# Kernel optimization log

Hardware: AMD Instinct MI355X
Metric: run time of the kernel (lower is better)

Reference implementation:

```python
import jax, jax.numpy as jnp
import numpy as np

CH = 96          # channels
E = 2 * CH       # expand_ratio * channels = 192
S = 16           # ssm_state_dim
LN_EPS = 1e-3    # keras LayerNormalization default epsilon


def setup_inputs() -> dict:
    key = jax.random.key(0)
    ks = jax.random.split(key, 8)
    inputs = jax.random.normal(ks[0], (8, 128, 128, CH), dtype=jnp.float32)
    scale = 0.05
    return {
        "inputs": inputs,
        "ln_gamma": jnp.ones((CH,), jnp.float32),
        "ln_beta": jnp.zeros((CH,), jnp.float32),
        "W_expand": jax.random.normal(ks[1], (CH, E), jnp.float32) * scale,
        "W_gate": jax.random.normal(ks[2], (CH, E), jnp.float32) * scale,
        "A": jax.random.normal(ks[3], (E, S), jnp.float32) * scale,
        "B": jax.random.normal(ks[4], (E, S), jnp.float32) * scale,
        "C": jax.random.normal(ks[5], (E, S), jnp.float32) * scale,
        "D": jnp.zeros((E,), jnp.float32),
        "W_out": jax.random.normal(ks[6], (E, CH), jnp.float32) * scale,
    }


def _layernorm(x, gamma, beta):
    mean = jnp.mean(x, axis=-1, keepdims=True)
    var = jnp.mean(jnp.square(x - mean), axis=-1, keepdims=True)
    return (x - mean) / jnp.sqrt(var + LN_EPS) * gamma + beta


def _ssm_scan(u, A, B, C, D):
    # u: [Bn, H, W, E]; diagonal linear recurrence along W with per-(channel,state) params.
    Bn, H, W, Ech = u.shape
    u_t = jnp.moveaxis(u, 2, 0)  # [W, Bn, H, E]

    def step(state, u_w):  # state: [Bn, H, E, S], u_w: [Bn, H, E]
        st = state * A + u_w[..., None] * B               # [Bn, H, E, S]
        # Faithful to the TF code: u*D is broadcast over the state dim
        # before the sum, contributing S * u * D.
        y = jnp.sum(st * C, axis=-1) + S * u_w * D        # [Bn, H, E]
        return st, y

    init = jnp.zeros((Bn, H, Ech, S), dtype=u.dtype)
    _, y = jax.lax.scan(step, init, u_t)                  # y: [W, Bn, H, E]
    return jnp.moveaxis(y, 0, 2)                          # [Bn, H, W, E]


def reference(inputs, ln_gamma, ln_beta, W_expand, W_gate, A, B, C, D, W_out):
    x = _layernorm(inputs, ln_gamma, ln_beta)
    x_proj = jnp.einsum("bhwc,ce->bhwe", x, W_expand)
    gate = jax.nn.sigmoid(jnp.einsum("bhwc,ce->bhwe", x, W_gate))
    ssm_out = _ssm_scan(x_proj, A, B, C, D)
    gated = gate * ssm_out
    return jnp.einsum("bhwe,ec->bhwc", gated, W_out)
```

## Files before the change

### kernel.cpp

```cpp
#include <hip/hip_runtime.h>
#include <math.h>

#define CHN 96
#define EC 192
#define SS 16
#define WPIX 128
#define TILE 16
#define NTILES (WPIX / TILE)
#define NT 192

__global__ __launch_bounds__(NT, 4)
void mamba_fused(const float* __restrict__ in,
                 const float* __restrict__ gamma,
                 const float* __restrict__ beta,
                 const float* __restrict__ We,
                 const float* __restrict__ Wg,
                 const float* __restrict__ Ap,
                 const float* __restrict__ Bp,
                 const float* __restrict__ Cp,
                 const float* __restrict__ Dp,
                 const float* __restrict__ Wo,
                 float* __restrict__ out) {
    __shared__ float xs[TILE][CHN];
    __shared__ float gs[TILE][EC];
    __shared__ float gsm[CHN], bsm[CHN];

    const int t = threadIdx.x;
    const int row = blockIdx.x;
    const float* inrow = in + (size_t)row * WPIX * CHN;

    if (t < CHN) { gsm[t] = gamma[t]; bsm[t] = beta[t]; }

    const int e = t;
    float Ar[SS], Br[SS], Cr[SS], st[SS];
    const float d = Dp[e];
    #pragma unroll
    for (int s4 = 0; s4 < SS / 4; ++s4) {
        float4 a = *(const float4*)&Ap[e * SS + s4 * 4];
        float4 b = *(const float4*)&Bp[e * SS + s4 * 4];
        float4 c = *(const float4*)&Cp[e * SS + s4 * 4];
        Ar[s4*4+0]=a.x; Ar[s4*4+1]=a.y; Ar[s4*4+2]=a.z; Ar[s4*4+3]=a.w;
        Br[s4*4+0]=b.x; Br[s4*4+1]=b.y; Br[s4*4+2]=b.z; Br[s4*4+3]=b.w;
        Cr[s4*4+0]=c.x; Cr[s4*4+1]=c.y; Cr[s4*4+2]=c.z; Cr[s4*4+3]=c.w;
    }
    #pragma unroll
    for (int s = 0; s < SS; ++s) st[s] = 0.f;

    const int px = t >> 3;
    const int ln = t & 7;
    const int co  = t % CHN;
    const int wgr = t / CHN;

    __syncthreads();

    for (int tile = 0; tile < NTILES; ++tile) {
        const int w0 = tile * TILE;

        if (t < 128) {
            const float* pin = inrow + (size_t)(w0 + px) * CHN + ln * 12;
            float4 v0 = *(const float4*)(pin + 0);
            float4 v1 = *(const float4*)(pin + 4);
            float4 v2 = *(const float4*)(pin + 8);
            float sum = v0.x + v0.y + v0.z + v0.w
                      + v1.x + v1.y + v1.z + v1.w
                      + v2.x + v2.y + v2.z + v2.w;
            float sq = v0.x*v0.x + v0.y*v0.y + v0.z*v0.z + v0.w*v0.w
                     + v1.x*v1.x + v1.y*v1.y + v1.z*v1.z + v1.w*v1.w
                     + v2.x*v2.x + v2.y*v2.y + v2.z*v2.z + v2.w*v2.w;
            #pragma unroll
            for (int m = 1; m < 8; m <<= 1) {
                sum += __shfl_xor(sum, m);
                sq  += __shfl_xor(sq,  m);
            }
            const float mean = sum * (1.f / CHN);
            const float var  = sq * (1.f / CHN) - mean * mean;
            const float rstd = rsqrtf(var + 1e-3f);
            const int cb = ln * 12;
            float o[12] = {v0.x,v0.y,v0.z,v0.w, v1.x,v1.y,v1.z,v1.w, v2.x,v2.y,v2.z,v2.w};
            #pragma unroll
            for (int k = 0; k < 12; ++k)
                o[k] = (o[k] - mean) * rstd * gsm[cb + k] + bsm[cb + k];
            *(float4*)&xs[px][cb + 0] = make_float4(o[0], o[1], o[2],  o[3]);
            *(float4*)&xs[px][cb + 4] = make_float4(o[4], o[5], o[6],  o[7]);
            *(float4*)&xs[px][cb + 8] = make_float4(o[8], o[9], o[10], o[11]);
        }
        __syncthreads();

        float accp[TILE], accg[TILE];
        #pragma unroll
        for (int w = 0; w < TILE; ++w) { accp[w] = 0.f; accg[w] = 0.f; }

        for (int c4 = 0; c4 < CHN / 4; ++c4) {
            const int c = c4 * 4;
            const float we0 = We[(c + 0) * EC + e];
            const float we1 = We[(c + 1) * EC + e];
            const float we2 = We[(c + 2) * EC + e];
            const float we3 = We[(c + 3) * EC + e];
            const float wg0 = Wg[(c + 0) * EC + e];
            const float wg1 = Wg[(c + 1) * EC + e];
            const float wg2 = Wg[(c + 2) * EC + e];
            const float wg3 = Wg[(c + 3) * EC + e];
            #pragma unroll
            for (int w = 0; w < TILE; ++w) {
                float4 xv = *(const float4*)&xs[w][c];
                accp[w] = fmaf(xv.x, we0, accp[w]);
                accp[w] = fmaf(xv.y, we1, accp[w]);
                accp[w] = fmaf(xv.z, we2, accp[w]);
                accp[w] = fmaf(xv.w, we3, accp[w]);
                accg[w] = fmaf(xv.x, wg0, accg[w]);
                accg[w] = fmaf(xv.y, wg1, accg[w]);
                accg[w] = fmaf(xv.z, wg2, accg[w]);
                accg[w] = fmaf(xv.w, wg3, accg[w]);
            }
        }

        #pragma unroll
        for (int w = 0; w < TILE; ++w) {
            const float u = accp[w];
            float y = (float)SS * u * d;
            #pragma unroll
            for (int s = 0; s < SS; ++s) {
                st[s] = fmaf(st[s], Ar[s], u * Br[s]);
                y = fmaf(st[s], Cr[s], y);
            }
            const float g = 1.f / (1.f + expf(-accg[w]));
            gs[w][e] = g * y;
        }
        __syncthreads();

        {
            float acco[8];
            #pragma unroll
            for (int j = 0; j < 8; ++j) acco[j] = 0.f;

            for (int e4 = 0; e4 < EC / 4; ++e4) {
                const int ee = e4 * 4;
                const float wo0 = Wo[(ee + 0) * CHN + co];
                const float wo1 = Wo[(ee + 1) * CHN + co];
                const float wo2 = Wo[(ee + 2) * CHN + co];
                const float wo3 = Wo[(ee + 3) * CHN + co];
                #pragma unroll
                for (int j = 0; j < 8; ++j) {
                    float4 gv = *(const float4*)&gs[wgr * 8 + j][ee];
                    acco[j] = fmaf(gv.x, wo0, acco[j]);
                    acco[j] = fmaf(gv.y, wo1, acco[j]);
                    acco[j] = fmaf(gv.z, wo2, acco[j]);
                    acco[j] = fmaf(gv.w, wo3, acco[j]);
                }
            }
            #pragma unroll
            for (int j = 0; j < 8; ++j) {
                out[((size_t)row * WPIX + w0 + wgr * 8 + j) * CHN + co] = acco[j];
            }
        }
        __syncthreads();
    }
}

extern "C" void kernel_launch(void* const* d_in, const int* in_sizes, int n_in,
                              void* d_out, int out_size, void* d_ws, size_t ws_size,
                              hipStream_t stream) {
    const float* in    = (const float*)d_in[0];
    const float* gamma = (const float*)d_in[1];
    const float* beta  = (const float*)d_in[2];
    const float* We    = (const float*)d_in[3];
    const float* Wg    = (const float*)d_in[4];
    const float* Ap    = (const float*)d_in[5];
    const float* Bp    = (const float*)d_in[6];
    const float* Cp    = (const float*)d_in[7];
    const float* Dp    = (const float*)d_in[8];
    const float* Wo    = (const float*)d_in[9];
    float* out = (float*)d_out;

    mamba_fused<<<dim3(8 * 128), dim3(NT), 0, stream>>>(
        in, gamma, beta, We, Wg, Ap, Bp, Cp, Dp, Wo, out);
}
```

Measured before the change: 438.3 us.

## Fold LayerNorm affine into projection weights and pipeline weight loads

Two small prep kernels pre-scale W_expand and W_gate by gamma and precompute per-channel column sums and beta terms. The fused kernel can then apply the normalization as a per-pixel rstd/mean correction after the matmul instead of normalizing every element. The projection now reads raw inputs straight from global memory (relying on cache broadcast) rather than staging normalized values in LDS. Weight loads for both matmuls are double-buffered in registers, the trailing barrier is dropped, the sigmoid uses __expf, and launch bounds drop to 3 waves. The trade-offs are repeated global/L1 reads of the input tile in place of LDS, higher register pressure, and slightly different rounding from the algebraic fold.

```diff
diff --git a/kernel.cpp b/kernel.cpp
--- a/kernel.cpp
+++ b/kernel.cpp
@@ -9,31 +9,98 @@
 #define NTILES (WPIX / TILE)
 #define NT 192
 
-__global__ __launch_bounds__(NT, 4)
+__global__ void prep_scale(const float* __restrict__ We,
+                           const float* __restrict__ Wg,
+                           const float* __restrict__ gamma,
+                           float* __restrict__ WeP,
+                           float* __restrict__ WgP) {
+    const int c = blockIdx.x;
+    const int e = threadIdx.x;
+    const float g = gamma[c];
+    WeP[c * EC + e] = g * We[c * EC + e];
+    WgP[c * EC + e] = g * Wg[c * EC + e];
+}
+
+__global__ void prep_sums(const float* __restrict__ We,
+                          const float* __restrict__ Wg,
+                          const float* __restrict__ beta,
+                          const float* __restrict__ WeP,
+                          const float* __restrict__ WgP,
+                          float* __restrict__ se, float* __restrict__ be,
+                          float* __restrict__ sg, float* __restrict__ bg) {
+    const int e = threadIdx.x;
+    float s1 = 0.f, b1 = 0.f, s2 = 0.f, b2 = 0.f;
+    for (int c = 0; c < CHN; ++c) {
+        s1 += WeP[c * EC + e];
+        s2 += WgP[c * EC + e];
+        b1 += beta[c] * We[c * EC + e];
+        b2 += beta[c] * Wg[c * EC + e];
+    }
+    se[e] = s1; be[e] = b1; sg[e] = s2; bg[e] = b2;
+}
+
+#define LOADW(W, c4) {                                         \
+    W##0 = wep[((c4) * 4 + 0) * EC]; W##1 = wep[((c4) * 4 + 1) * EC]; \
+    W##2 = wep[((c4) * 4 + 2) * EC]; W##3 = wep[((c4) * 4 + 3) * EC]; \
+    W##4 = wgp[((c4) * 4 + 0) * EC]; W##5 = wgp[((c4) * 4 + 1) * EC]; \
+    W##6 = wgp[((c4) * 4 + 2) * EC]; W##7 = wgp[((c4) * 4 + 3) * EC]; }
+
+#define FMAB(W, c4) {                                          \
+    _Pragma("unroll")                                          \
+    for (int w = 0; w < TILE; ++w) {                           \
+        float4 xv = *(const float4*)(xtile + w * CHN + (c4) * 4); \
+        accp[w] = fmaf(xv.x, W##0, accp[w]);                   \
+        accp[w] = fmaf(xv.y, W##1, accp[w]);                   \
+        accp[w] = fmaf(xv.z, W##2, accp[w]);                   \
+        accp[w] = fmaf(xv.w, W##3, accp[w]);                   \
+        accg[w] = fmaf(xv.x, W##4, accg[w]);                   \
+        accg[w] = fmaf(xv.y, W##5, accg[w]);                   \
+        accg[w] = fmaf(xv.z, W##6, accg[w]);                   \
+        accg[w] = fmaf(xv.w, W##7, accg[w]); } }
+
+#define LOADO(W, ch) {                                         \
+    _Pragma("unroll")                                          \
+    for (int k = 0; k < 16; ++k) W[k] = Wo[((ch) * 16 + k) * CHN + co]; }
+
+#define FMAO(W, ch) {                                          \
+    _Pragma("unroll")                                          \
+    for (int j = 0; j < 8; ++j) {                              \
+        const float* gp_ = &gs[wgr * 8 + j][(ch) * 16];        \
+        _Pragma("unroll")                                      \
+        for (int k4 = 0; k4 < 4; ++k4) {                       \
+            float4 gv = *(const float4*)(gp_ + k4 * 4);        \
+            acco[j] = fmaf(gv.x, W[k4 * 4 + 0], acco[j]);      \
+            acco[j] = fmaf(gv.y, W[k4 * 4 + 1], acco[j]);      \
+            acco[j] = fmaf(gv.z, W[k4 * 4 + 2], acco[j]);      \
+            acco[j] = fmaf(gv.w, W[k4 * 4 + 3], acco[j]); } } }
+
+__global__ __launch_bounds__(NT, 3)
 void mamba_fused(const float* __restrict__ in,
-                 const float* __restrict__ gamma,
-                 const float* __restrict__ beta,
-                 const float* __restrict__ We,
-                 const float* __restrict__ Wg,
+                 const float* __restrict__ WeP,
+                 const float* __restrict__ WgP,
+                 const float* __restrict__ sev,
+                 const float* __restrict__ bev,
+                 const float* __restrict__ sgv,
+                 const float* __restrict__ bgv,
                  const float* __restrict__ Ap,
                  const float* __restrict__ Bp,
                  const float* __restrict__ Cp,
                  const float* __restrict__ Dp,
                  const float* __restrict__ Wo,
                  float* __restrict__ out) {
-    __shared__ float xs[TILE][CHN];
     __shared__ float gs[TILE][EC];
-    __shared__ float gsm[CHN], bsm[CHN];
+    __shared__ float2 stats[TILE];
 
     const int t = threadIdx.x;
     const int row = blockIdx.x;
     const float* inrow = in + (size_t)row * WPIX * CHN;
 
-    if (t < CHN) { gsm[t] = gamma[t]; bsm[t] = beta[t]; }
-
     const int e = t;
+    const float* wep = WeP + e;
+    const float* wgp = WgP + e;
     float Ar[SS], Br[SS], Cr[SS], st[SS];
-    const float d = Dp[e];
+    const float dd = Dp[e];
+    const float se_r = sev[e], be_r = bev[e], sg_r = sgv[e], bg_r = bgv[e];
     #pragma unroll
     for (int s4 = 0; s4 < SS / 4; ++s4) {
         float4 a = *(const float4*)&Ap[e * SS + s4 * 4];
@@ -46,18 +113,17 @@
     #pragma unroll
     for (int s = 0; s < SS; ++s) st[s] = 0.f;
 
-    const int px = t >> 3;
-    const int ln = t & 7;
+    const int px  = t >> 3;
+    const int ln  = t & 7;
     const int co  = t % CHN;
     const int wgr = t / CHN;
 
-    __syncthreads();
-
     for (int tile = 0; tile < NTILES; ++tile) {
         const int w0 = tile * TILE;
+        const float* xtile = inrow + (size_t)w0 * CHN;
 
         if (t < 128) {
-            const float* pin = inrow + (size_t)(w0 + px) * CHN + ln * 12;
+            const float* pin = xtile + (size_t)px * CHN + ln * 12;
             float4 v0 = *(const float4*)(pin + 0);
             float4 v1 = *(const float4*)(pin + 4);
             float4 v2 = *(const float4*)(pin + 8);
@@ -75,14 +141,7 @@
             const float mean = sum * (1.f / CHN);
             const float var  = sq * (1.f / CHN) - mean * mean;
             const float rstd = rsqrtf(var + 1e-3f);
-            const int cb = ln * 12;
-            float o[12] = {v0.x,v0.y,v0.z,v0.w, v1.x,v1.y,v1.z,v1.w, v2.x,v2.y,v2.z,v2.w};
-            #pragma unroll
-            for (int k = 0; k < 12; ++k)
-                o[k] = (o[k] - mean) * rstd * gsm[cb + k] + bsm[cb + k];
-            *(float4*)&xs[px][cb + 0] = make_float4(o[0], o[1], o[2],  o[3]);
-            *(float4*)&xs[px][cb + 4] = make_float4(o[4], o[5], o[6],  o[7]);
-            *(float4*)&xs[px][cb + 8] = make_float4(o[8], o[9], o[10], o[11]);
+            if (ln == 0) stats[px] = make_float2(rstd, mean * rstd);
         }
         __syncthreads();
 
@@ -90,40 +149,31 @@
         #pragma unroll
         for (int w = 0; w < TILE; ++w) { accp[w] = 0.f; accg[w] = 0.f; }
 
-        for (int c4 = 0; c4 < CHN / 4; ++c4) {
-            const int c = c4 * 4;
-            const float we0 = We[(c + 0) * EC + e];
-            const float we1 = We[(c + 1) * EC + e];
-            const float we2 = We[(c + 2) * EC + e];
-            const float we3 = We[(c + 3) * EC + e];
-            const float wg0 = Wg[(c + 0) * EC + e];
-            const float wg1 = Wg[(c + 1) * EC + e];
-            const float wg2 = Wg[(c + 2) * EC + e];
-            const float wg3 = Wg[(c + 3) * EC + e];
-            #pragma unroll
-            for (int w = 0; w < TILE; ++w) {
-                float4 xv = *(const float4*)&xs[w][c];
-                accp[w] = fmaf(xv.x, we0, accp[w]);
-                accp[w] = fmaf(xv.y, we1, accp[w]);
-                accp[w] = fmaf(xv.z, we2, accp[w]);
-                accp[w] = fmaf(xv.w, we3, accp[w]);
-                accg[w] = fmaf(xv.x, wg0, accg[w]);
-                accg[w] = fmaf(xv.y, wg1, accg[w]);
-                accg[w] = fmaf(xv.z, wg2, accg[w]);
-                accg[w] = fmaf(xv.w, wg3, accg[w]);
+        {
+            float wA0, wA1, wA2, wA3, wA4, wA5, wA6, wA7;
+            float wB0, wB1, wB2, wB3, wB4, wB5, wB6, wB7;
+            LOADW(wA, 0);
+            for (int c4 = 0; c4 < 24; c4 += 2) {
+                LOADW(wB, c4 + 1);
+                FMAB(wA, c4);
+                const int nx = (c4 + 2 < 24) ? c4 + 2 : 0;
+                LOADW(wA, nx);
+                FMAB(wB, c4 + 1);
             }
         }
 
         #pragma unroll
         for (int w = 0; w < TILE; ++w) {
-            const float u = accp[w];
-            float y = (float)SS * u * d;
+            const float2 sp = stats[w];
+            const float u  = fmaf(accp[w], sp.x, fmaf(-sp.y, se_r, be_r));
+            const float gp = fmaf(accg[w], sp.x, fmaf(-sp.y, sg_r, bg_r));
+            float y = (float)SS * u * dd;
             #pragma unroll
             for (int s = 0; s < SS; ++s) {
                 st[s] = fmaf(st[s], Ar[s], u * Br[s]);
                 y = fmaf(st[s], Cr[s], y);
             }
-            const float g = 1.f / (1.f + expf(-accg[w]));
+            const float g = 1.f / (1.f + __expf(-gp));
             gs[w][e] = g * y;
         }
         __syncthreads();
@@ -133,27 +183,21 @@
             #pragma unroll
             for (int j = 0; j < 8; ++j) acco[j] = 0.f;
 
-            for (int e4 = 0; e4 < EC / 4; ++e4) {
-                const int ee = e4 * 4;
-                const float wo0 = Wo[(ee + 0) * CHN + co];
-                const float wo1 = Wo[(ee + 1) * CHN + co];
-                const float wo2 = Wo[(ee + 2) * CHN + co];
-                const float wo3 = Wo[(ee + 3) * CHN + co];
-                #pragma unroll
-                for (int j = 0; j < 8; ++j) {
-                    float4 gv = *(const float4*)&gs[wgr * 8 + j][ee];
-                    acco[j] = fmaf(gv.x, wo0, acco[j]);
-                    acco[j] = fmaf(gv.y, wo1, acco[j]);
-                    acco[j] = fmaf(gv.z, wo2, acco[j]);
-                    acco[j] = fmaf(gv.w, wo3, acco[j]);
-                }
-            }
+            float WA[16], WB[16];
+            LOADO(WA, 0);
+            for (int ch = 0; ch < 12; ch += 2) {
+                LOADO(WB, ch + 1);
+                FMAO(WA, ch);
+                const int nx = (ch + 2 < 12) ? ch + 2 : 0;
+                LOADO(WA, nx);
+                FMAO(WB, ch + 1);
+            }
+
             #pragma unroll
             for (int j = 0; j < 8; ++j) {
                 out[((size_t)row * WPIX + w0 + wgr * 8 + j) * CHN + co] = acco[j];
             }
         }
-        __syncthreads();
     }
 }
 
@@ -172,6 +216,16 @@
     const float* Wo    = (const float*)d_in[9];
     float* out = (float*)d_out;
 
+    float* wsf = (float*)d_ws;
+    float* WeP = wsf;
+    float* WgP = wsf + 18432;
+    float* se  = wsf + 36864;
+    float* be  = wsf + 37056;
+    float* sg  = wsf + 37248;
+    float* bg  = wsf + 37440;
+
+    prep_scale<<<dim3(CHN), dim3(EC), 0, stream>>>(We, Wg, gamma, WeP, WgP);
+    prep_sums<<<dim3(1), dim3(EC), 0, stream>>>(We, Wg, beta, WeP, WgP, se, be, sg, bg);
     mamba_fused<<<dim3(8 * 128), dim3(NT), 0, stream>>>(
-        in, gamma, beta, We, Wg, Ap, Bp, Cp, Dp, Wo, out);
-}
+        in, WeP, WgP, se, be, sg, bg, Ap, Bp, Cp, Dp, Wo, out);
+}
```

Measured after the change: 358.0 us. 18.3% less time.
